# Optimization experiments

Hardware: AMD Instinct MI355X
Metric: run time of the kernel (lower is better)

Reference implementation:

```python
import jax, jax.numpy as jnp
import numpy as np

INPUT_DIM = 256
OUTPUT_DIM = 256
DEGREE = 7


def setup_inputs() -> dict:
    key = jax.random.key(0)
    k1, k2 = jax.random.split(key)
    x = jax.random.normal(k1, (16, 2048, INPUT_DIM), dtype=jnp.float32)
    std = 1.0 / (INPUT_DIM * (DEGREE + 1))
    hermite_coeffs = std * jax.random.normal(k2, (INPUT_DIM, OUTPUT_DIM, DEGREE + 1), dtype=jnp.float32)
    return {"x": x, "hermite_coeffs": hermite_coeffs}


def reference(x, hermite_coeffs):
    a, b, c = x.shape
    degree = hermite_coeffs.shape[2] - 1
    xf = jnp.tanh(x.reshape(-1, c))  # [N, input_dim]
    hs = [jnp.ones_like(xf)]
    if degree > 0:
        hs.append(2.0 * xf)
    for i in range(2, degree + 1):
        hs.append(2.0 * xf * hs[-1] - 2.0 * (i - 1) * hs[-2])
    hermite = jnp.stack(hs, axis=-1)  # [N, input_dim, degree+1]
    y = jnp.einsum('bid,iod->bo', hermite, hermite_coeffs)
    return y.reshape(a, b, hermite_coeffs.shape[1])
```

## Files before the change

kernel.cpp:

```cpp
#include <hip/hip_runtime.h>
#include <hip/hip_bf16.h>
#include <math.h>

#define INPUT_DIM 256
#define OUT_DIM   256
#define NDEG      8
#define KTOT      (INPUT_DIM * NDEG)
#define NROWS     (16 * 2048)

#define BM  64
#define BN  256
#define BK  64
#define NK  (KTOT / BK)
#define LDT 72
#define CHUNK_ELEMS 16384

typedef __bf16 bf16x8 __attribute__((ext_vector_type(8)));
typedef float  f32x4  __attribute__((ext_vector_type(4)));

__global__ __launch_bounds__(256) void reorder_coeffs(const float* __restrict__ C,
                                                      __bf16* __restrict__ Bt) {
    int g = blockIdx.x * 256 + threadIdx.x;
    int i = g >> 8;
    int o = g & 255;
    const float4* src = (const float4*)(C + (size_t)i * (OUT_DIM * NDEG) + o * NDEG);
    float4 a = src[0];
    float4 b = src[1];
    bf16x8 v;
    v[0] = (__bf16)a.x; v[1] = (__bf16)a.y; v[2] = (__bf16)a.z; v[3] = (__bf16)a.w;
    v[4] = (__bf16)b.x; v[5] = (__bf16)b.y; v[6] = (__bf16)b.z; v[7] = (__bf16)b.w;
    int kc = i >> 3;
    int p  = i & 7;
    size_t dst = (size_t)kc * CHUNK_ELEMS + p * 2048 + o * 8;
    *(bf16x8*)(Bt + dst) = v;
}

__global__ __launch_bounds__(512, 4) void hermite_mfma(const float* __restrict__ x,
                                                       const __bf16* __restrict__ Bt,
                                                       float* __restrict__ out) {
    __shared__ __align__(16) __bf16 Alds[BM * LDT];
    __shared__ __align__(16) __bf16 Blds[CHUNK_ELEMS];

    const int tid  = threadIdx.x;
    const int bm   = blockIdx.x;
    const int wave = tid >> 6;
    const int lane = tid & 63;
    const int wr   = (wave >> 2) * 32;
    const int wc   = (wave & 3) * 64;
    const int lrow = lane & 15;
    const int quad = lane >> 4;

    const int am = tid >> 3;
    const int ah = tid & 7;
    const float* xptr = x + (size_t)(bm * BM + am) * INPUT_DIM + ah;

    const int wbase = wave * 2048 + lane * 8;

    f32x4 acc[2][4] = {};

    for (int kc = 0; kc < NK; ++kc) {
        float xs = xptr[kc * 8];

        const __bf16* gsrc = Bt + (size_t)kc * CHUNK_ELEMS + wbase;
        #pragma unroll
        for (int i = 0; i < 4; ++i) {
            __builtin_amdgcn_global_load_lds(
                (const __attribute__((address_space(1))) void*)(gsrc + i * 512),
                (__attribute__((address_space(3))) void*)(&Blds[wbase + i * 512]),
                16, 0, 0);
        }

        {
            float e = __expf(2.0f * xs);
            float t = 1.0f - 2.0f / (e + 1.0f);
            bf16x8 v;
            float hm2 = 1.0f;
            float hm1 = 2.0f * t;
            v[0] = (__bf16)hm2;
            v[1] = (__bf16)hm1;
            #pragma unroll
            for (int d = 2; d < 8; ++d) {
                float h = 2.0f * t * hm1 - 2.0f * (float)(d - 1) * hm2;
                v[d] = (__bf16)h;
                hm2 = hm1; hm1 = h;
            }
            *(bf16x8*)(&Alds[am * LDT + ah * 8]) = v;
        }

        __syncthreads();

        #pragma unroll
        for (int ki = 0; ki < 2; ++ki) {
            bf16x8 af[2], bfr[4];
            #pragma unroll
            for (int mi = 0; mi < 2; ++mi)
                af[mi] = *(const bf16x8*)(&Alds[(wr + mi * 16 + lrow) * LDT + ki * 32 + quad * 8]);
            #pragma unroll
            for (int ni = 0; ni < 4; ++ni)
                bfr[ni] = *(const bf16x8*)(&Blds[(ki * 4 + quad) * 2048 + (wc + ni * 16 + lrow) * 8]);
            #pragma unroll
            for (int mi = 0; mi < 2; ++mi)
                #pragma unroll
                for (int ni = 0; ni < 4; ++ni)
                    acc[mi][ni] = __builtin_amdgcn_mfma_f32_16x16x32_bf16(
                        af[mi], bfr[ni], acc[mi][ni], 0, 0, 0);
        }

        __syncthreads();
    }

    #pragma unroll
    for (int mi = 0; mi < 2; ++mi) {
        #pragma unroll
        for (int r = 0; r < 4; ++r) {
            int row = bm * BM + wr + mi * 16 + quad * 4 + r;
            float* orow = out + (size_t)row * OUT_DIM + wc + lrow;
            #pragma unroll
            for (int ni = 0; ni < 4; ++ni)
                orow[ni * 16] = acc[mi][ni][r];
        }
    }
}

extern "C" void kernel_launch(void* const* d_in, const int* in_sizes, int n_in,
                              void* d_out, int out_size, void* d_ws, size_t ws_size,
                              hipStream_t stream) {
    const float* x = (const float*)d_in[0];
    const float* C = (const float*)d_in[1];
    float* out = (float*)d_out;
    __bf16* Bt = (__bf16*)d_ws;

    reorder_coeffs<<<dim3((INPUT_DIM * OUT_DIM) / 256), dim3(256), 0, stream>>>(C, Bt);
    hermite_mfma<<<dim3(NROWS / BM), dim3(512), 0, stream>>>(x, Bt, out);
}
```

Measured before the change: 121.6 us.

## Double-buffer A and B tiles in LDS and prefetch next chunk

Adds ping-pong LDS buffers for the Hermite-feature A tile and the coefficient B tile. The next chunk's global-to-LDS loads and featurization are issued before the MFMAs on the current chunk, which removes one barrier per iteration and hides load latency. It also changes the A tile layout to be k-major (lane indexes rows, wave indexes input feature), so global x reads are strided differently. LDS use roughly doubles, which may cut occupancy.

```diff
diff --git a/kernel.cpp b/kernel.cpp
--- a/kernel.cpp
+++ b/kernel.cpp
@@ -12,8 +12,8 @@
 #define BN  256
 #define BK  64
 #define NK  (KTOT / BK)
-#define LDT 72
-#define CHUNK_ELEMS 16384
+#define ACH 4096
+#define BCH 16384
 
 typedef __bf16 bf16x8 __attribute__((ext_vector_type(8)));
 typedef float  f32x4  __attribute__((ext_vector_type(4)));
@@ -31,15 +31,15 @@
     v[4] = (__bf16)b.x; v[5] = (__bf16)b.y; v[6] = (__bf16)b.z; v[7] = (__bf16)b.w;
     int kc = i >> 3;
     int p  = i & 7;
-    size_t dst = (size_t)kc * CHUNK_ELEMS + p * 2048 + o * 8;
+    size_t dst = (size_t)kc * BCH + p * 2048 + o * 8;
     *(bf16x8*)(Bt + dst) = v;
 }
 
 __global__ __launch_bounds__(512, 4) void hermite_mfma(const float* __restrict__ x,
                                                        const __bf16* __restrict__ Bt,
                                                        float* __restrict__ out) {
-    __shared__ __align__(16) __bf16 Alds[BM * LDT];
-    __shared__ __align__(16) __bf16 Blds[CHUNK_ELEMS];
+    __shared__ __align__(16) __bf16 Alds[2][ACH];
+    __shared__ __align__(16) __bf16 Blds[2][BCH];
 
     const int tid  = threadIdx.x;
     const int bm   = blockIdx.x;
@@ -50,54 +50,71 @@
     const int lrow = lane & 15;
     const int quad = lane >> 4;
 
-    const int am = tid >> 3;
-    const int ah = tid & 7;
-    const float* xptr = x + (size_t)(bm * BM + am) * INPUT_DIM + ah;
+    const float* xp = x + (size_t)(bm * BM + lane) * INPUT_DIM + wave;
 
     const int wbase = wave * 2048 + lane * 8;
 
     f32x4 acc[2][4] = {};
 
+#define FEATURIZE(XS, DST)                                                  \
+    {                                                                       \
+        float e = __expf(2.0f * (XS));           \
+        float t = 1.0f - 2.0f / (e + 1.0f);                                 \
+        bf16x8 v;                                                           \
+        float hm2 = 1.0f;                                          \
+        float hm1 = 2.0f * t;                                      \
+        v[0] = (__bf16)hm2;                                                 \
+        v[1] = (__bf16)hm1;                                                 \
+        _Pragma("unroll")                                                   \
+        for (int d = 2; d < 8; ++d) {                                       \
+            float h = 2.0f * t * hm1 - 2.0f * (float)(d - 1) * hm2;         \
+            v[d] = (__bf16)h;                                               \
+            hm2 = hm1; hm1 = h;                                             \
+        }                                                                   \
+        *(bf16x8*)(DST) = v;                                                \
+    }
+
+    float xs = xp[0];
+    {
+        const __bf16* g = Bt + wbase;
+        #pragma unroll
+        for (int i = 0; i < 4; ++i)
+            __builtin_amdgcn_global_load_lds(
+                (const __attribute__((address_space(1))) void*)(g + i * 512),
+                (__attribute__((address_space(3))) void*)(&Blds[0][wbase + i * 512]),
+                16, 0, 0);
+    }
+    FEATURIZE(xs, &Alds[0][tid * 8]);
+    xs = xp[8];
+    __syncthreads();
+
     for (int kc = 0; kc < NK; ++kc) {
-        float xs = xptr[kc * 8];
+        const int buf  = kc & 1;
+        const int nbuf = buf ^ 1;
 
-        const __bf16* gsrc = Bt + (size_t)kc * CHUNK_ELEMS + wbase;
-        #pragma unroll
-        for (int i = 0; i < 4; ++i) {
-            __builtin_amdgcn_global_load_lds(
-                (const __attribute__((address_space(1))) void*)(gsrc + i * 512),
-                (__attribute__((address_space(3))) void*)(&Blds[wbase + i * 512]),
-                16, 0, 0);
+        if (kc + 1 < NK) {
+            const __bf16* g = Bt + (size_t)(kc + 1) * BCH + wbase;
+            #pragma unroll
+            for (int i = 0; i < 4; ++i)
+                __builtin_amdgcn_global_load_lds(
+                    (const __attribute__((address_space(1))) void*)(g + i * 512),
+                    (__attribute__((address_space(3))) void*)(&Blds[nbuf][wbase + i * 512]),
+                    16, 0, 0);
+
+            FEATURIZE(xs, &Alds[nbuf][tid * 8]);
+            int kn = (kc + 2 < NK) ? kc + 2 : NK - 1;
+            xs = xp[kn * 8];
         }
-
-        {
-            float e = __expf(2.0f * xs);
-            float t = 1.0f - 2.0f / (e + 1.0f);
-            bf16x8 v;
-            float hm2 = 1.0f;
-            float hm1 = 2.0f * t;
-            v[0] = (__bf16)hm2;
-            v[1] = (__bf16)hm1;
-            #pragma unroll
-            for (int d = 2; d < 8; ++d) {
-                float h = 2.0f * t * hm1 - 2.0f * (float)(d - 1) * hm2;
-                v[d] = (__bf16)h;
-                hm2 = hm1; hm1 = h;
-            }
-            *(bf16x8*)(&Alds[am * LDT + ah * 8]) = v;
-        }
-
-        __syncthreads();
 
         #pragma unroll
         for (int ki = 0; ki < 2; ++ki) {
             bf16x8 af[2], bfr[4];
             #pragma unroll
             for (int mi = 0; mi < 2; ++mi)
-                af[mi] = *(const bf16x8*)(&Alds[(wr + mi * 16 + lrow) * LDT + ki * 32 + quad * 8]);
+                af[mi] = *(const bf16x8*)(&Alds[buf][((ki * 4 + quad) * 64 + wr + mi * 16 + lrow) * 8]);
             #pragma unroll
             for (int ni = 0; ni < 4; ++ni)
-                bfr[ni] = *(const bf16x8*)(&Blds[(ki * 4 + quad) * 2048 + (wc + ni * 16 + lrow) * 8]);
+                bfr[ni] = *(const bf16x8*)(&Blds[buf][((ki * 4 + quad) * 256 + wc + ni * 16 + lrow) * 8]);
             #pragma unroll
             for (int mi = 0; mi < 2; ++mi)
                 #pragma unroll
@@ -120,6 +137,7 @@
                 orow[ni * 16] = acc[mi][ni][r];
         }
     }
+#undef FEATURIZE
 }
 
 extern "C" void kernel_launch(void* const* d_in, const int* in_sizes, int n_in,
```

After: 124.0 us. Within noise of the previous version (+1.9%).

## Double-buffer per-wave B slices, compute A fragments in registers, use 32x32 MFMA

Applied to the files above, without the earlier changes.

Restructures the GEMM so each of 4 waves owns a private 64-column slice of B in LDS, double-buffered with async global-to-LDS loads, which removes both block-wide barriers per K step. The Hermite features are computed directly into MFMA A-operand registers instead of going through an LDS tile. Each wave now covers all 64 rows, and the instruction changes from 16x16x32 to 32x32x16. The cost is more register pressure, featurization repeated in every wave, and a waitcnt encoding that has to be exactly right for the async copy.

```diff
diff --git a/kernel.cpp b/kernel.cpp
--- a/kernel.cpp
+++ b/kernel.cpp
@@ -9,20 +9,18 @@
 #define NROWS     (16 * 2048)
 
 #define BM  64
-#define BN  256
 #define BK  64
 #define NK  (KTOT / BK)
-#define LDT 72
-#define CHUNK_ELEMS 16384
+#define SLICE 4096
 
 typedef __bf16 bf16x8 __attribute__((ext_vector_type(8)));
-typedef float  f32x4  __attribute__((ext_vector_type(4)));
+typedef float  f32x16 __attribute__((ext_vector_type(16)));
 
 __global__ __launch_bounds__(256) void reorder_coeffs(const float* __restrict__ C,
                                                       __bf16* __restrict__ Bt) {
-    int g = blockIdx.x * 256 + threadIdx.x;
-    int i = g >> 8;
-    int o = g & 255;
+    int g_ = blockIdx.x * 256 + threadIdx.x;
+    int i = g_ >> 8;
+    int o = g_ & 255;
     const float4* src = (const float4*)(C + (size_t)i * (OUT_DIM * NDEG) + o * NDEG);
     float4 a = src[0];
     float4 b = src[1];
@@ -31,95 +29,112 @@
     v[4] = (__bf16)b.x; v[5] = (__bf16)b.y; v[6] = (__bf16)b.z; v[7] = (__bf16)b.w;
     int kc = i >> 3;
     int p  = i & 7;
-    size_t dst = (size_t)kc * CHUNK_ELEMS + p * 2048 + o * 8;
+    int g  = o >> 6;
+    int ol = o & 63;
+    size_t dst = (size_t)kc * (4 * SLICE) + g * SLICE + p * 512 + ol * 8;
     *(bf16x8*)(Bt + dst) = v;
 }
 
-__global__ __launch_bounds__(512, 4) void hermite_mfma(const float* __restrict__ x,
+__device__ __forceinline__ bf16x8 featurize(float xs) {
+    float e = __expf(2.0f * xs);
+    float t = 1.0f - 2.0f / (e + 1.0f);
+    bf16x8 v;
+    float hm2 = 1.0f;
+    float hm1 = 2.0f * t;
+    v[0] = (__bf16)hm2;
+    v[1] = (__bf16)hm1;
+    #pragma unroll
+    for (int d = 2; d < 8; ++d) {
+        float h = 2.0f * t * hm1 - 2.0f * (float)(d - 1) * hm2;
+        v[d] = (__bf16)h;
+        hm2 = hm1; hm1 = h;
+    }
+    return v;
+}
+
+__global__ __launch_bounds__(256, 2) void hermite_mfma(const float* __restrict__ x,
                                                        const __bf16* __restrict__ Bt,
                                                        float* __restrict__ out) {
-    __shared__ __align__(16) __bf16 Alds[BM * LDT];
-    __shared__ __align__(16) __bf16 Blds[CHUNK_ELEMS];
+    __shared__ __align__(16) __bf16 Blds[4 * 2 * SLICE];
 
     const int tid  = threadIdx.x;
     const int bm   = blockIdx.x;
     const int wave = tid >> 6;
     const int lane = tid & 63;
-    const int wr   = (wave >> 2) * 32;
-    const int wc   = (wave & 3) * 64;
-    const int lrow = lane & 15;
-    const int quad = lane >> 4;
+    const int l31  = lane & 31;
+    const int h    = lane >> 5;
 
-    const int am = tid >> 3;
-    const int ah = tid & 7;
-    const float* xptr = x + (size_t)(bm * BM + am) * INPUT_DIM + ah;
+    const float* xr0 = x + (size_t)(bm * BM + l31) * INPUT_DIM + h;
+    const float* xr1 = xr0 + 32 * INPUT_DIM;
 
-    const int wbase = wave * 2048 + lane * 8;
+    const __bf16* bsrc = Bt + (size_t)wave * SLICE + lane * 8;
+    __bf16* bl = &Blds[wave * 2 * SLICE];
+    const int loff = lane * 8;
 
-    f32x4 acc[2][4] = {};
+    f32x16 acc[2][2] = {};
+
+    float xs0[4], xs1[4];
+    #pragma unroll
+    for (int s = 0; s < 4; ++s) { xs0[s] = xr0[2 * s]; xs1[s] = xr1[2 * s]; }
+    #pragma unroll
+    for (int i = 0; i < 8; ++i)
+        __builtin_amdgcn_global_load_lds(
+            (const __attribute__((address_space(1))) void*)(bsrc + i * 512),
+            (__attribute__((address_space(3))) void*)(bl + i * 512 + loff),
+            16, 0, 0);
 
     for (int kc = 0; kc < NK; ++kc) {
-        float xs = xptr[kc * 8];
+        const int buf = kc & 1;
 
-        const __bf16* gsrc = Bt + (size_t)kc * CHUNK_ELEMS + wbase;
+        bf16x8 af0[4], af1[4];
         #pragma unroll
-        for (int i = 0; i < 4; ++i) {
-            __builtin_amdgcn_global_load_lds(
-                (const __attribute__((address_space(1))) void*)(gsrc + i * 512),
-                (__attribute__((address_space(3))) void*)(&Blds[wbase + i * 512]),
-                16, 0, 0);
+        for (int s = 0; s < 4; ++s) { af0[s] = featurize(xs0[s]); af1[s] = featurize(xs1[s]); }
+
+        __builtin_amdgcn_s_waitcnt(0x0f70);
+
+        bf16x8 bfr[4][2];
+        #pragma unroll
+        for (int s = 0; s < 4; ++s)
+            #pragma unroll
+            for (int ni = 0; ni < 2; ++ni)
+                bfr[s][ni] = *(const bf16x8*)(bl + buf * SLICE + (2 * s + h) * 512
+                                              + (ni * 32 + l31) * 8);
+
+        if (kc + 1 < NK) {
+            const __bf16* g = bsrc + (size_t)(kc + 1) * (4 * SLICE);
+            #pragma unroll
+            for (int i = 0; i < 8; ++i)
+                __builtin_amdgcn_global_load_lds(
+                    (const __attribute__((address_space(1))) void*)(g + i * 512),
+                    (__attribute__((address_space(3))) void*)(bl + (buf ^ 1) * SLICE + i * 512 + loff),
+                    16, 0, 0);
+            #pragma unroll
+            for (int s = 0; s < 4; ++s) {
+                xs0[s] = xr0[(kc + 1) * 8 + 2 * s];
+                xs1[s] = xr1[(kc + 1) * 8 + 2 * s];
+            }
         }
 
-        {
-            float e = __expf(2.0f * xs);
-            float t = 1.0f - 2.0f / (e + 1.0f);
-            bf16x8 v;
-            float hm2 = 1.0f;
-            float hm1 = 2.0f * t;
-            v[0] = (__bf16)hm2;
-            v[1] = (__bf16)hm1;
-            #pragma unroll
-            for (int d = 2; d < 8; ++d) {
-                float h = 2.0f * t * hm1 - 2.0f * (float)(d - 1) * hm2;
-                v[d] = (__bf16)h;
-                hm2 = hm1; hm1 = h;
-            }
-            *(bf16x8*)(&Alds[am * LDT + ah * 8]) = v;
+        #pragma unroll
+        for (int s = 0; s < 4; ++s) {
+            acc[0][0] = __builtin_amdgcn_mfma_f32_32x32x16_bf16(af0[s], bfr[s][0], acc[0][0], 0, 0, 0);
+            acc[0][1] = __builtin_amdgcn_mfma_f32_32x32x16_bf16(af0[s], bfr[s][1], acc[0][1], 0, 0, 0);
+            acc[1][0] = __builtin_amdgcn_mfma_f32_32x32x16_bf16(af1[s], bfr[s][0], acc[1][0], 0, 0, 0);
+            acc[1][1] = __builtin_amdgcn_mfma_f32_32x32x16_bf16(af1[s], bfr[s][1], acc[1][1], 0, 0, 0);
         }
-
-        __syncthreads();
-
-        #pragma unroll
-        for (int ki = 0; ki < 2; ++ki) {
-            bf16x8 af[2], bfr[4];
-            #pragma unroll
-            for (int mi = 0; mi < 2; ++mi)
-                af[mi] = *(const bf16x8*)(&Alds[(wr + mi * 16 + lrow) * LDT + ki * 32 + quad * 8]);
-            #pragma unroll
-            for (int ni = 0; ni < 4; ++ni)
-                bfr[ni] = *(const bf16x8*)(&Blds[(ki * 4 + quad) * 2048 + (wc + ni * 16 + lrow) * 8]);
-            #pragma unroll
-            for (int mi = 0; mi < 2; ++mi)
-                #pragma unroll
-                for (int ni = 0; ni < 4; ++ni)
-                    acc[mi][ni] = __builtin_amdgcn_mfma_f32_16x16x32_bf16(
-                        af[mi], bfr[ni], acc[mi][ni], 0, 0, 0);
-        }
-
-        __syncthreads();
     }
 
     #pragma unroll
-    for (int mi = 0; mi < 2; ++mi) {
+    for (int mi = 0; mi < 2; ++mi)
         #pragma unroll
-        for (int r = 0; r < 4; ++r) {
-            int row = bm * BM + wr + mi * 16 + quad * 4 + r;
-            float* orow = out + (size_t)row * OUT_DIM + wc + lrow;
+        for (int ni = 0; ni < 2; ++ni) {
             #pragma unroll
-            for (int ni = 0; ni < 4; ++ni)
-                orow[ni * 16] = acc[mi][ni][r];
+            for (int r = 0; r < 16; ++r) {
+                int rl  = (r & 3) + 8 * (r >> 2) + 4 * h;
+                int row = bm * BM + mi * 32 + rl;
+                out[(size_t)row * OUT_DIM + wave * 64 + ni * 32 + l31] = acc[mi][ni][r];
+            }
         }
-    }
 }
 
 extern "C" void kernel_launch(void* const* d_in, const int* in_sizes, int n_in,
@@ -131,5 +146,5 @@
     __bf16* Bt = (__bf16*)d_ws;
 
     reorder_coeffs<<<dim3((INPUT_DIM * OUT_DIM) / 256), dim3(256), 0, stream>>>(C, Bt);
-    hermite_mfma<<<dim3(NROWS / BM), dim3(512), 0, stream>>>(x, Bt, out);
+    hermite_mfma<<<dim3(NROWS / BM), dim3(256), 0, stream>>>(x, Bt, out);
 }
```

Result: slower. 155.6 us (+27.9%).
